# Performance work log

Hardware: AMD Instinct MI355X
Metric: run time of the kernel (lower is better)

Reference implementation:

```python
import jax, jax.numpy as jnp
import numpy as np

N_BATCHES = 32
N_LABELS = 100


def setup_inputs() -> dict:
    key = jax.random.key(0)
    ks = jax.random.split(key, 7)
    N, D, P = 16384, 2048, 256
    x = jax.random.normal(ks[0], (N, D), dtype=jnp.float32)
    label = jax.random.randint(ks[1], (N,), 0, N_LABELS, dtype=jnp.int64)
    label_batch = jnp.sort(jax.random.randint(ks[2], (N,), 0, N_BATCHES, dtype=jnp.int64))
    W1_w = jax.random.normal(ks[3], (P, D), dtype=jnp.float32) * 0.02
    W1_b = jax.random.normal(ks[4], (P,), dtype=jnp.float32) * 0.02
    W2_w = jax.random.normal(ks[5], (P, D), dtype=jnp.float32) * 0.02
    W2_b = jax.random.normal(ks[6], (P,), dtype=jnp.float32) * 0.02
    return {"x": x, "label": label, "label_batch": label_batch,
            "W1_w": W1_w, "W1_b": W1_b, "W2_w": W2_w, "W2_b": W2_b}


def _loo_diff_label_mean(x, label, label_batch):
    # For each sample i: mean of x over {j : label_batch[j]==label_batch[i] and label[j]!=label[i]}.
    # Rows with no such j are zero (torch code's `continue`). x is detached in the original.
    N = x.shape[0]
    xs = jax.lax.stop_gradient(x)
    seg = label_batch * N_LABELS + label                      # combined (group,label) key
    n_seg = N_BATCHES * N_LABELS
    ones = jnp.ones((N,), dtype=x.dtype)
    sum_bl = jax.ops.segment_sum(xs, seg, num_segments=n_seg)            # [n_seg, D]
    cnt_bl = jax.ops.segment_sum(ones, seg, num_segments=n_seg)          # [n_seg]
    sum_b = jax.ops.segment_sum(xs, label_batch, num_segments=N_BATCHES)  # [NB, D]
    cnt_b = jax.ops.segment_sum(ones, label_batch, num_segments=N_BATCHES)
    diff_sum = sum_b[label_batch] - sum_bl[seg]               # [N, D]
    diff_cnt = cnt_b[label_batch] - cnt_bl[seg]               # [N]
    safe = jnp.maximum(diff_cnt, 1.0)
    mean = diff_sum / safe[:, None]
    return jnp.where((diff_cnt > 0)[:, None], mean, jnp.zeros_like(mean))


def reference(x, label, label_batch, W1_w, W1_b, W2_w, W2_b):
    calc_mean = _loo_diff_label_mean(x, label, label_batch)   # detached aggregate
    return x @ W1_w.T + W1_b + calc_mean @ W2_w.T + W2_b      # W1(x) + W2(mean)
```

## Files before the change

### kernel.cpp

```cpp
#include <hip/hip_runtime.h>
#include <cstdint>

#define N_SAMPLES 16384
#define DIM 2048
#define PDIM 256
#define NB 32
#define NL 100
#define NSEG (NB * NL)

typedef float floatx4 __attribute__((ext_vector_type(4)));
typedef __bf16 bf16x8 __attribute__((ext_vector_type(8)));

__device__ __forceinline__ unsigned short f32_to_bf16(float f) {
    unsigned int u = __float_as_uint(f);
    u += 0x7fffu + ((u >> 16) & 1u);
    return (unsigned short)(u >> 16);
}
__device__ __forceinline__ unsigned int pack_bf16x2(float a, float b) {
    return (unsigned int)f32_to_bf16(a) | ((unsigned int)f32_to_bf16(b) << 16);
}

__global__ __launch_bounds__(256) void prep_kernel(
    const float* __restrict__ W1w, const float* __restrict__ W1b,
    const float* __restrict__ W2w, const float* __restrict__ W2b,
    const int* __restrict__ label, const int* __restrict__ lbatch,
    unsigned short* __restrict__ W1bf, unsigned short* __restrict__ W2bf,
    float* __restrict__ bias, int* __restrict__ seg,
    int* __restrict__ hist, float* __restrict__ SW2)
{
    int i = blockIdx.x * 256 + threadIdx.x;
    W1bf[i] = f32_to_bf16(W1w[i]);
    W2bf[i] = f32_to_bf16(W2w[i]);
    if (i < PDIM) bias[i] = W1b[i] + W2b[i];
    if (i < N_SAMPLES) seg[i] = lbatch[i] * NL + label[i];
    if (i < NSEG) hist[i] = 0;
    if (i < NSEG * PDIM / 2) ((float2*)SW2)[i] = make_float2(0.f, 0.f);
}

__global__ __launch_bounds__(256) void hist_kernel(
    const int* __restrict__ seg, int* __restrict__ hist)
{
    int i = blockIdx.x * 256 + threadIdx.x;
    atomicAdd(&hist[seg[i]], 1);
}

#define SCAN_BPT 13
__global__ __launch_bounds__(256) void scan_kernel(
    const int* __restrict__ hist, int* __restrict__ offs, int* __restrict__ cursor)
{
    __shared__ int ps[256];
    const int t = threadIdx.x;
    int local = 0;
    #pragma unroll
    for (int k = 0; k < SCAN_BPT; ++k) {
        int bin = t * SCAN_BPT + k;
        if (bin < NSEG) local += hist[bin];
    }
    ps[t] = local;
    __syncthreads();
    for (int d = 1; d < 256; d <<= 1) {
        int v = (t >= d) ? ps[t - d] : 0;
        __syncthreads();
        ps[t] += v;
        __syncthreads();
    }
    int run = ps[t] - local;
    #pragma unroll
    for (int k = 0; k < SCAN_BPT; ++k) {
        int bin = t * SCAN_BPT + k;
        if (bin < NSEG) {
            offs[bin] = run;
            cursor[bin] = run;
            run += hist[bin];
        }
    }
    if (t == 255) offs[NSEG] = ps[255];
}

__global__ __launch_bounds__(256) void scatter_kernel(
    const int* __restrict__ seg, int* __restrict__ cursor, int* __restrict__ perm)
{
    int i = blockIdx.x * 256 + threadIdx.x;
    int pos = atomicAdd(&cursor[seg[i]], 1);
    perm[pos] = i;
}

__global__ __launch_bounds__(256) void segsum_kernel(
    const float* __restrict__ x, const int* __restrict__ perm,
    const int* __restrict__ offs,
    unsigned short* __restrict__ xb, unsigned short* __restrict__ sumb)
{
    const int tid = threadIdx.x;
    const int w = tid >> 6, lane = tid & 63;
    const int s = blockIdx.y * 4 + w;
    const int c = blockIdx.x * 512 + lane * 8;
    const int beg = offs[s], end = offs[s + 1];

    floatx4 sum0 = {0.f, 0.f, 0.f, 0.f};
    floatx4 sum1 = {0.f, 0.f, 0.f, 0.f};
    for (int base = beg; base < end; base += 64) {
        int p = (base + lane < end) ? perm[base + lane] : 0;
        const int n = min(end - base, 64);
        for (int j0 = 0; j0 < n; j0 += 8) {
            int rr[8];
            floatx4 v0[8], v1[8];
            #pragma unroll
            for (int j = 0; j < 8; ++j) {
                rr[j] = __shfl(p, min(j0 + j, n - 1));
                const float* px = &x[(size_t)rr[j] * DIM + c];
                v0[j] = *(const floatx4*)px;
                v1[j] = *(const floatx4*)(px + 4);
            }
            #pragma unroll
            for (int j = 0; j < 8; ++j) {
                if (j < n - j0) {
                    sum0 += v0[j];
                    sum1 += v1[j];
                    uint4 o;
                    o.x = pack_bf16x2(v0[j][0], v0[j][1]);
                    o.y = pack_bf16x2(v0[j][2], v0[j][3]);
                    o.z = pack_bf16x2(v1[j][0], v1[j][1]);
                    o.w = pack_bf16x2(v1[j][2], v1[j][3]);
                    *(uint4*)&xb[(size_t)rr[j] * DIM + c] = o;
                }
            }
        }
    }
    uint4 so;
    so.x = pack_bf16x2(sum0[0], sum0[1]);
    so.y = pack_bf16x2(sum0[2], sum0[3]);
    so.z = pack_bf16x2(sum1[0], sum1[1]);
    so.w = pack_bf16x2(sum1[2], sum1[3]);
    *(uint4*)&sumb[(size_t)s * DIM + c] = so;
}

__global__ __launch_bounds__(256) void finalize_kernel(
    float* __restrict__ SW2, const int* __restrict__ offs)
{
    const int b = blockIdx.x;
    const int col = threadIdx.x;
    const int cb = offs[(b + 1) * NL] - offs[b * NL];
    float tot = 0.f;
    #pragma unroll 4
    for (int l = 0; l < NL; ++l)
        tot += SW2[(size_t)(b * NL + l) * PDIM + col];
    for (int l = 0; l < NL; ++l) {
        const int s = b * NL + l;
        const int dc = cb - (offs[s + 1] - offs[s]);
        const float v = SW2[(size_t)s * PDIM + col];
        SW2[(size_t)s * PDIM + col] = (dc > 0) ? (tot - v) / (float)dc : 0.f;
    }
}

template<int BM, int BN, int WR, int WC, bool FUSE, int KSPLIT>
__global__ __launch_bounds__(256) void gemm_bt_kernel(
    const unsigned short* __restrict__ A,
    const unsigned short* __restrict__ B,
    float* __restrict__ C,
    const float* __restrict__ bias,
    const float* __restrict__ add,
    const int* __restrict__ seg,
    int K)
{
    constexpr int SM = BM / WR, SN = BN / WC;
    constexpr int FM = SM / 16, FN = SN / 16;
    __shared__ __align__(16) unsigned short ldsA[BM * 32];
    __shared__ __align__(16) unsigned short ldsB[BN * 32];
    const int tid = threadIdx.x;
    const int lane = tid & 63;
    const int wave = tid >> 6;
    const int wr = wave / WC, wc = wave % WC;
    const int quad = lane >> 4, l15 = lane & 15;
    const int m0 = blockIdx.x * BM;
    const int n0 = blockIdx.y * BN;
    const int kpw = K / KSPLIT;
    const int k0 = blockIdx.z * kpw;
    const int srow = lane >> 2, schunk = lane & 3;

    floatx4 acc[FM][FN];
    #pragma unroll
    for (int i = 0; i < FM; ++i)
        #pragma unroll
        for (int j = 0; j < FN; ++j) acc[i][j] = (floatx4){0.f, 0.f, 0.f, 0.f};

    const unsigned short* Abase = A + (size_t)(m0 + srow) * K + schunk * 8;
    const unsigned short* Bbase = B + (size_t)(n0 + srow) * K + schunk * 8;

    for (int kk = k0; kk < k0 + kpw; kk += 32) {
        __syncthreads();
        #pragma unroll
        for (int ch = wave; ch < BM / 16; ch += 4)
            __builtin_amdgcn_global_load_lds(
                (const __attribute__((address_space(1))) void*)(Abase + (size_t)ch * 16 * K + kk),
                (__attribute__((address_space(3))) void*)&ldsA[ch * 16 * 32], 16, 0, 0);
        #pragma unroll
        for (int ch = wave; ch < BN / 16; ch += 4)
            __builtin_amdgcn_global_load_lds(
                (const __attribute__((address_space(1))) void*)(Bbase + (size_t)ch * 16 * K + kk),
                (__attribute__((address_space(3))) void*)&ldsB[ch * 16 * 32], 16, 0, 0);
        __syncthreads();

        bf16x8 af[FM], bfr[FN];
        #pragma unroll
        for (int mi = 0; mi < FM; ++mi)
            af[mi] = *(const bf16x8*)&ldsA[(wr * SM + mi * 16 + l15) * 32 + quad * 8];
        #pragma unroll
        for (int ni = 0; ni < FN; ++ni)
            bfr[ni] = *(const bf16x8*)&ldsB[(wc * SN + ni * 16 + l15) * 32 + quad * 8];
        #pragma unroll
        for (int mi = 0; mi < FM; ++mi)
            #pragma unroll
            for (int ni = 0; ni < FN; ++ni)
                acc[mi][ni] = __builtin_amdgcn_mfma_f32_16x16x32_bf16(
                    af[mi], bfr[ni], acc[mi][ni], 0, 0, 0);
    }

    #pragma unroll
    for (int mi = 0; mi < FM; ++mi) {
        const int rbase = m0 + wr * SM + mi * 16 + quad * 4;
        #pragma unroll
        for (int ni = 0; ni < FN; ++ni) {
            const int col = n0 + wc * SN + ni * 16 + l15;
            float bsum = 0.f;
            if constexpr (FUSE) bsum = bias[col];
            #pragma unroll
            for (int r = 0; r < 4; ++r) {
                const int row = rbase + r;
                float v = acc[mi][ni][r];
                if constexpr (FUSE) v += bsum + add[(size_t)seg[row] * PDIM + col];
                if constexpr (KSPLIT > 1)
                    atomicAdd(&C[(size_t)row * PDIM + col], v);
                else
                    C[(size_t)row * PDIM + col] = v;
            }
        }
    }
}

extern "C" void kernel_launch(void* const* d_in, const int* in_sizes, int n_in,
                              void* d_out, int out_size, void* d_ws, size_t ws_size,
                              hipStream_t stream)
{
    const float* x      = (const float*)d_in[0];
    const int*   label  = (const int*)d_in[1];
    const int*   lbatch = (const int*)d_in[2];
    const float* W1w    = (const float*)d_in[3];
    const float* W1b    = (const float*)d_in[4];
    const float* W2w    = (const float*)d_in[5];
    const float* W2b    = (const float*)d_in[6];
    float* out = (float*)d_out;

    char* ws = (char*)d_ws;
    size_t off = 0;
    auto alloc = [&](size_t bytes) {
        void* p = ws + off;
        off = (off + bytes + 255) & ~(size_t)255;
        return p;
    };
    unsigned short* xb   = (unsigned short*)alloc((size_t)N_SAMPLES * DIM * 2);
    unsigned short* sumb = (unsigned short*)alloc((size_t)NSEG * DIM * 2);
    unsigned short* W1bf = (unsigned short*)alloc((size_t)PDIM * DIM * 2);
    unsigned short* W2bf = (unsigned short*)alloc((size_t)PDIM * DIM * 2);
    float* SW2    = (float*)alloc((size_t)NSEG * PDIM * 4);
    float* bias   = (float*)alloc(PDIM * 4);
    int*   seg    = (int*)alloc(N_SAMPLES * 4);
    int*   perm   = (int*)alloc(N_SAMPLES * 4);
    int*   hist   = (int*)alloc(NSEG * 4);
    int*   offs   = (int*)alloc((NSEG + 1) * 4);
    int*   cursor = (int*)alloc(NSEG * 4);

    prep_kernel<<<PDIM * DIM / 256, 256, 0, stream>>>(
        W1w, W1b, W2w, W2b, label, lbatch, W1bf, W2bf, bias, seg, hist, SW2);

    hist_kernel<<<N_SAMPLES / 256, 256, 0, stream>>>(seg, hist);
    scan_kernel<<<1, 256, 0, stream>>>(hist, offs, cursor);
    scatter_kernel<<<N_SAMPLES / 256, 256, 0, stream>>>(seg, cursor, perm);

    segsum_kernel<<<dim3(DIM / 512, NSEG / 4), 256, 0, stream>>>(
        x, perm, offs, xb, sumb);

    gemm_bt_kernel<32, 256, 1, 4, false, 2>
        <<<dim3(NSEG / 32, 1, 2), 256, 0, stream>>>(
        sumb, W2bf, SW2, nullptr, nullptr, nullptr, DIM);

    finalize_kernel<<<NB, 256, 0, stream>>>(SW2, offs);

    gemm_bt_kernel<64, 128, 2, 2, true, 1>
        <<<dim3(N_SAMPLES / 64, PDIM / 128), 256, 0, stream>>>(
        xb, W1bf, out, bias, SW2, seg, DIM);
}
```

Before: 316.3 us.

## Double-buffer GEMM LDS tiles, fold histogram into scan, raise K-split

The GEMM kernel now double-buffers its LDS tiles, issuing the next K-slice's global-to-LDS loads before the current slice's MFMAs, with one barrier per iteration instead of two. The separate global-atomic histogram kernel is removed and the histogram is built in shared memory inside the single-block scan kernel, saving a launch. The segment-sum GEMM's K-split goes from 2 to 4 for more parallelism, at the cost of more output atomics. The risks are doubled LDS use lowering occupancy, and a serialized single-block histogram over all samples.

```diff
diff --git a/kernel.cpp b/kernel.cpp
--- a/kernel.cpp
+++ b/kernel.cpp
@@ -26,35 +26,35 @@
     const int* __restrict__ label, const int* __restrict__ lbatch,
     unsigned short* __restrict__ W1bf, unsigned short* __restrict__ W2bf,
     float* __restrict__ bias, int* __restrict__ seg,
-    int* __restrict__ hist, float* __restrict__ SW2)
+    float* __restrict__ SW2)
 {
     int i = blockIdx.x * 256 + threadIdx.x;
     W1bf[i] = f32_to_bf16(W1w[i]);
     W2bf[i] = f32_to_bf16(W2w[i]);
     if (i < PDIM) bias[i] = W1b[i] + W2b[i];
     if (i < N_SAMPLES) seg[i] = lbatch[i] * NL + label[i];
-    if (i < NSEG) hist[i] = 0;
     if (i < NSEG * PDIM / 2) ((float2*)SW2)[i] = make_float2(0.f, 0.f);
-}
-
-__global__ __launch_bounds__(256) void hist_kernel(
-    const int* __restrict__ seg, int* __restrict__ hist)
-{
-    int i = blockIdx.x * 256 + threadIdx.x;
-    atomicAdd(&hist[seg[i]], 1);
 }
 
 #define SCAN_BPT 13
 __global__ __launch_bounds__(256) void scan_kernel(
-    const int* __restrict__ hist, int* __restrict__ offs, int* __restrict__ cursor)
-{
+    const int* __restrict__ seg, int* __restrict__ offs, int* __restrict__ cursor)
+{
+    __shared__ int lh[NSEG];
     __shared__ int ps[256];
     const int t = threadIdx.x;
+    for (int i = t; i < NSEG; i += 256) lh[i] = 0;
+    __syncthreads();
+    #pragma unroll 4
+    for (int i = t; i < N_SAMPLES; i += 256)
+        atomicAdd(&lh[seg[i]], 1);
+    __syncthreads();
+
     int local = 0;
     #pragma unroll
     for (int k = 0; k < SCAN_BPT; ++k) {
         int bin = t * SCAN_BPT + k;
-        if (bin < NSEG) local += hist[bin];
+        if (bin < NSEG) local += lh[bin];
     }
     ps[t] = local;
     __syncthreads();
@@ -71,7 +71,7 @@
         if (bin < NSEG) {
             offs[bin] = run;
             cursor[bin] = run;
-            run += hist[bin];
+            run += lh[bin];
         }
     }
     if (t == 255) offs[NSEG] = ps[255];
@@ -164,8 +164,8 @@
 {
     constexpr int SM = BM / WR, SN = BN / WC;
     constexpr int FM = SM / 16, FN = SN / 16;
-    __shared__ __align__(16) unsigned short ldsA[BM * 32];
-    __shared__ __align__(16) unsigned short ldsB[BN * 32];
+    __shared__ __align__(16) unsigned short ldsA[2][BM * 32];
+    __shared__ __align__(16) unsigned short ldsB[2][BN * 32];
     const int tid = threadIdx.x;
     const int lane = tid & 63;
     const int wave = tid >> 6;
@@ -186,33 +186,42 @@
     const unsigned short* Abase = A + (size_t)(m0 + srow) * K + schunk * 8;
     const unsigned short* Bbase = B + (size_t)(n0 + srow) * K + schunk * 8;
 
-    for (int kk = k0; kk < k0 + kpw; kk += 32) {
-        __syncthreads();
+    auto stage = [&](int buf, int kk) {
         #pragma unroll
         for (int ch = wave; ch < BM / 16; ch += 4)
             __builtin_amdgcn_global_load_lds(
                 (const __attribute__((address_space(1))) void*)(Abase + (size_t)ch * 16 * K + kk),
-                (__attribute__((address_space(3))) void*)&ldsA[ch * 16 * 32], 16, 0, 0);
+                (__attribute__((address_space(3))) void*)&ldsA[buf][ch * 16 * 32], 16, 0, 0);
         #pragma unroll
         for (int ch = wave; ch < BN / 16; ch += 4)
             __builtin_amdgcn_global_load_lds(
                 (const __attribute__((address_space(1))) void*)(Bbase + (size_t)ch * 16 * K + kk),
-                (__attribute__((address_space(3))) void*)&ldsB[ch * 16 * 32], 16, 0, 0);
-        __syncthreads();
+                (__attribute__((address_space(3))) void*)&ldsB[buf][ch * 16 * 32], 16, 0, 0);
+    };
+
+    const int nt = kpw / 32;
+    stage(0, k0);
+    __syncthreads();
+
+    for (int t = 0; t < nt; ++t) {
+        const int cur = t & 1;
+        if (t + 1 < nt) stage(cur ^ 1, k0 + (t + 1) * 32);
 
         bf16x8 af[FM], bfr[FN];
         #pragma unroll
         for (int mi = 0; mi < FM; ++mi)
-            af[mi] = *(const bf16x8*)&ldsA[(wr * SM + mi * 16 + l15) * 32 + quad * 8];
+            af[mi] = *(const bf16x8*)&ldsA[cur][(wr * SM + mi * 16 + l15) * 32 + quad * 8];
         #pragma unroll
         for (int ni = 0; ni < FN; ++ni)
-            bfr[ni] = *(const bf16x8*)&ldsB[(wc * SN + ni * 16 + l15) * 32 + quad * 8];
+            bfr[ni] = *(const bf16x8*)&ldsB[cur][(wc * SN + ni * 16 + l15) * 32 + quad * 8];
         #pragma unroll
         for (int mi = 0; mi < FM; ++mi)
             #pragma unroll
             for (int ni = 0; ni < FN; ++ni)
                 acc[mi][ni] = __builtin_amdgcn_mfma_f32_16x16x32_bf16(
                     af[mi], bfr[ni], acc[mi][ni], 0, 0, 0);
+
+        __syncthreads();
     }
 
     #pragma unroll
@@ -265,22 +274,20 @@
     float* bias   = (float*)alloc(PDIM * 4);
     int*   seg    = (int*)alloc(N_SAMPLES * 4);
     int*   perm   = (int*)alloc(N_SAMPLES * 4);
-    int*   hist   = (int*)alloc(NSEG * 4);
     int*   offs   = (int*)alloc((NSEG + 1) * 4);
     int*   cursor = (int*)alloc(NSEG * 4);
 
     prep_kernel<<<PDIM * DIM / 256, 256, 0, stream>>>(
-        W1w, W1b, W2w, W2b, label, lbatch, W1bf, W2bf, bias, seg, hist, SW2);
-
-    hist_kernel<<<N_SAMPLES / 256, 256, 0, stream>>>(seg, hist);
-    scan_kernel<<<1, 256, 0, stream>>>(hist, offs, cursor);
+        W1w, W1b, W2w, W2b, label, lbatch, W1bf, W2bf, bias, seg, SW2);
+
+    scan_kernel<<<1, 256, 0, stream>>>(seg, offs, cursor);
     scatter_kernel<<<N_SAMPLES / 256, 256, 0, stream>>>(seg, cursor, perm);
 
     segsum_kernel<<<dim3(DIM / 512, NSEG / 4), 256, 0, stream>>>(
         x, perm, offs, xb, sumb);
 
-    gemm_bt_kernel<32, 256, 1, 4, false, 2>
-        <<<dim3(NSEG / 32, 1, 2), 256, 0, stream>>>(
+    gemm_bt_kernel<32, 256, 1, 4, false, 4>
+        <<<dim3(NSEG / 32, 1, 4), 256, 0, stream>>>(
         sumb, W2bf, SW2, nullptr, nullptr, nullptr, DIM);
 
     finalize_kernel<<<NB, 256, 0, stream>>>(SW2, offs);
```

After: 324.1 us. 2.5% more time.
